# Optimization experiments

Hardware: AMD Instinct MI355X
Metric: run time of the kernel (lower is better)

## Reference

```python
import jax, jax.numpy as jnp
import numpy as np

N = 100000; E = 1600000; G = 2000; S = 40; MAXP = 50
IN = 64; F = 128; H = 4; HD = F // H; FFN = 8 * F
EPS = 1e-5; BN_EPS = 1e-5

def _ln(x, g, b):
    m = jnp.mean(x, -1, keepdims=True)
    v = jnp.mean((x - m) ** 2, -1, keepdims=True)
    return (x - m) * jax.lax.rsqrt(v + EPS) * g + b

def setup_inputs():
    key = jax.random.key(0)
    ks = jax.random.split(key, 16)
    def lin(k, i, o):
        kw, kb = jax.random.split(k)
        lim = 1.0 / np.sqrt(i)
        return (jax.random.uniform(kw, (i, o), jnp.float32, -lim, lim),
                jax.random.uniform(kb, (o,), jnp.float32, -lim, lim))
    W_gcn, b_gcn = lin(ks[1], IN, F)
    Wq, bq = lin(ks[2], F, F); Wk, bk = lin(ks[3], F, F)
    Wv, bv = lin(ks[4], F, F); Wo, bo = lin(ks[5], F, F)
    W1, b1 = lin(ks[6], F, FFN); W2, b2 = lin(ks[7], FFN, F)
    Wg, bg = lin(ks[8], 2 * F, F)
    ones = lambda: jnp.ones((F,), jnp.float32)
    zeros = lambda: jnp.zeros((F,), jnp.float32)
    return {
        'x': jax.random.normal(ks[0], (N, IN), jnp.float32),
        'edge_index': jax.random.randint(ks[9], (2, E), 0, N),
        'batch': jnp.repeat(jnp.arange(G), N // G),
        'set_batch': jnp.repeat(jnp.arange(S), G // S),
        'W_gcn': W_gcn, 'b_gcn': b_gcn,
        'bn_g': ones(), 'bn_b': zeros(),
        'lnpre_g': ones(), 'lnpre_b': zeros(),
        'Wq': Wq, 'bq': bq, 'Wk': Wk, 'bk': bk, 'Wv': Wv, 'bv': bv, 'Wo': Wo, 'bo': bo,
        'ln1_g': ones(), 'ln1_b': zeros(),
        'W1': W1, 'b1': b1, 'W2': W2, 'b2': b2,
        'ln2_g': ones(), 'ln2_b': zeros(),
        'Wg': Wg, 'bg': bg,
    }

def _forward(x, W_gcn, b_gcn, bn_g, bn_b, lnpre_g, lnpre_b, Wq, bq, Wk, bk, Wv, bv, Wo, bo, ln1_g, ln1_b, W1, b1, W2, b2, ln2_g, ln2_b, Wg, bg, edge_index, batch, set_batch):
    row, col = edge_index[0], edge_index[1]
    # GCNConv, improved=True -> self-loop weight 2.0 (PyG gcn_norm)
    xw = x @ W_gcn                                              # [N,F]
    deg = jax.ops.segment_sum(jnp.ones(E, xw.dtype), col, N) + 2.0
    dinv = jax.lax.rsqrt(deg)
    norm = dinv[row] * dinv[col]                                # [E]
    agg = jax.ops.segment_sum(xw[row] * norm[:, None], col, N)  # scatter-add to targets
    h = agg + (2.0 * dinv * dinv)[:, None] * xw + b_gcn
    # BatchNorm1d eval (running_mean=0, running_var=1) + ReLU; dropout is identity in eval
    h = jax.nn.relu(h * jax.lax.rsqrt(jnp.asarray(1.0 + BN_EPS, h.dtype)) * bn_g + bn_b)
    # global mean pool per graph
    cnt_g = jax.ops.segment_sum(jnp.ones(N, h.dtype), batch, G)
    z = jax.ops.segment_sum(h, batch, G) / cnt_g[:, None]       # [G,F]
    # to_dense_batch over sets (set_batch is sorted)
    cnt_s = jax.ops.segment_sum(jnp.ones(G, jnp.int32), set_batch, S)
    starts = jnp.cumsum(cnt_s) - cnt_s
    pos = jnp.arange(G) - starts[set_batch]                     # position within set
    zd = jnp.zeros((S, MAXP, F), z.dtype).at[set_batch, pos].set(z)
    mask = jnp.arange(MAXP)[None, :] < cnt_s[:, None]           # [S,MAXP]
    # pre-LN MHA with key_padding_mask
    zn = _ln(zd, lnpre_g, lnpre_b)
    q = (zn @ Wq + bq).reshape(S, MAXP, H, HD)
    k = (zn @ Wk + bk).reshape(S, MAXP, H, HD)
    v = (zn @ Wv + bv).reshape(S, MAXP, H, HD)
    scores = jnp.einsum('sqhd,skhd->shqk', q, k) / np.sqrt(HD)
    scores = jnp.where(mask[:, None, None, :], scores, -1e9)
    attn = jax.nn.softmax(scores, -1)
    o = jnp.einsum('shqk,skhd->sqhd', attn, v).reshape(S, MAXP, F) @ Wo + bo
    zd = _ln(zd + o, ln1_g, ln1_b)
    # FFN block (post-LN residual)
    f = jax.nn.relu(zd @ W1 + b1) @ W2 + b2
    zd = _ln(zd + f, ln2_g, ln2_b)
    # z_dense[mask] ordering == gather via (set_batch, pos); broadcast to nodes
    set_info = zd[set_batch, pos][batch]                        # [N,F]
    # gated fusion
    gate = jax.nn.sigmoid(jnp.concatenate([h, set_info], -1) @ Wg + bg)
    return gate * set_info + (1.0 - gate) * h

def reference(x, edge_index, batch, set_batch, W_gcn, b_gcn, bn_g, bn_b, lnpre_g, lnpre_b, Wq, bq, Wk, bk, Wv, bv, Wo, bo, ln1_g, ln1_b, W1, b1, W2, b2, ln2_g, ln2_b, Wg, bg):
    return _forward(x, W_gcn, b_gcn, bn_g, bn_b, lnpre_g, lnpre_b, Wq, bq, Wk, bk, Wv, bv, Wo, bo, ln1_g, ln1_b, W1, b1, W2, b2, ln2_g, ln2_b, Wg, bg, edge_index, batch, set_batch)
```

## Files before the change

kernel.cpp:

```cpp
#include <hip/hip_runtime.h>
#include <hip/hip_bf16.h>
#include <cstddef>

#define NN 100000
#define NE 1600000
#define NG 2000
#define NS 40
#define INF 64
#define F 128
#define FFN_DIM 1024
#define NB 782
#define BCAP 3072
#define SC_BLOCKS 512
#define SC_CHUNK 3125

using bf16 = __hip_bfloat16;
typedef __attribute__((ext_vector_type(8))) short short8;
typedef __attribute__((ext_vector_type(4))) float f32x4;
typedef __attribute__((ext_vector_type(2))) float f32x2;

__device__ __forceinline__ short f2bs(float f){
    union { bf16 b; short s; } u; u.b = __float2bfloat16(f); return u.s;
}
__device__ __forceinline__ unsigned int pk2(float a, float b){
    return (unsigned int)(unsigned short)f2bs(a) | ((unsigned int)(unsigned short)f2bs(b) << 16);
}

__global__ __launch_bounds__(1024) void k_init(int* __restrict__ bcursor, const float* __restrict__ Wg,
                                               unsigned short* __restrict__ Wgb){
    int t = threadIdx.x;
    if (t < NB) bcursor[t] = t * BCAP;
    for (int i=t; i<16384; i+=1024){
        int k = i >> 7, n = i & 127;
        Wgb[n*128 + k] = (unsigned short)f2bs(Wg[(size_t)k*F + n]);
    }
}

__global__ __launch_bounds__(256) void k_xws(const float* __restrict__ x, const float* __restrict__ W,
                                             const float* __restrict__ dinv, unsigned char* __restrict__ xws8){
    __shared__ short Xs[128*72];
    __shared__ short Ws[128*72];
    int t = threadIdx.x;
    int rowBase = blockIdx.x * 128;
    #pragma unroll
    for (int i=0;i<32;i++){
        int id = i*256+t; int k = id>>7, n = id&127;
        Ws[n*72 + k] = f2bs(W[id]);
    }
    #pragma unroll
    for (int i=0;i<8;i++){
        int id = i*256+t;
        int r = id>>4; int k4 = (id&15)*4;
        int row = rowBase + r; if (row >= NN) row = NN-1;
        float4 v = *(const float4*)&x[(size_t)row*INF + k4];
        *(unsigned int*)&Xs[r*72 + k4]     = pk2(v.x, v.y);
        *(unsigned int*)&Xs[r*72 + k4 + 2] = pk2(v.z, v.w);
    }
    __syncthreads();
    int lane = t & 63, w = t >> 6;
    int lr = lane & 15, quad = lane >> 4;
    f32x4 acc[2][8];
    #pragma unroll
    for (int i=0;i<2;i++)
        #pragma unroll
        for (int j=0;j<8;j++) acc[i][j] = (f32x4){0.f,0.f,0.f,0.f};
    #pragma unroll
    for (int ks=0; ks<2; ++ks){
        int kb = ks*32 + quad*8;
        short8 b0 = *(const short8*)&Xs[((w  )*16 + lr)*72 + kb];
        short8 b1 = *(const short8*)&Xs[((w+4)*16 + lr)*72 + kb];
        #pragma unroll
        for (int mt=0; mt<8; ++mt){
            short8 a = *(const short8*)&Ws[(mt*16 + lr)*72 + kb];
            acc[0][mt] = __builtin_amdgcn_mfma_f32_16x16x32_bf16(a, b0, acc[0][mt], 0, 0, 0);
            acc[1][mt] = __builtin_amdgcn_mfma_f32_16x16x32_bf16(a, b1, acc[1][mt], 0, 0, 0);
        }
    }
    #pragma unroll
    for (int rt=0; rt<2; ++rt){
        int row = rowBase + (w + rt*4)*16 + lr;
        if (row < NN){
            float dv = dinv[row];
            #pragma unroll
            for (int mt=0; mt<8; ++mt){
                int p = __builtin_amdgcn_cvt_pk_fp8_f32(acc[rt][mt][0]*dv, acc[rt][mt][1]*dv, 0, false);
                p     = __builtin_amdgcn_cvt_pk_fp8_f32(acc[rt][mt][2]*dv, acc[rt][mt][3]*dv, p, true);
                *(int*)&xws8[(size_t)row*F + mt*16 + quad*4] = p;
            }
        }
    }
}

__global__ __launch_bounds__(1024) void k_scatter2(const int* __restrict__ ei, int* __restrict__ bcursor,
                                                   int* __restrict__ ebuf){
    __shared__ int lh[NB];
    __shared__ int lb[NB];
    int t = threadIdx.x;
    int base = blockIdx.x * SC_CHUNK;
    for (int b=t; b<NB; b+=1024) lh[b] = 0;
    __syncthreads();
    int rr[4], cc[4];
    #pragma unroll
    for (int q=0;q<4;q++){
        int i = t + q*1024;
        bool v = (i < SC_CHUNK);
        int idx = v ? (base + i) : base;
        rr[q] = ei[idx];
        cc[q] = ei[NE + idx];
        if (v) atomicAdd(&lh[cc[q]>>7], 1);
    }
    __syncthreads();
    for (int b=t; b<NB; b+=1024){
        int n = lh[b];
        lb[b] = n ? atomicAdd(&bcursor[b], n) : 0;
        lh[b] = 0;
    }
    __syncthreads();
    #pragma unroll
    for (int q=0;q<4;q++){
        int i = t + q*1024;
        if (i < SC_CHUNK){
            int b = cc[q] >> 7;
            int rk = atomicAdd(&lh[b], 1);
            ebuf[lb[b] + rk] = (rr[q] << 7) | (cc[q] & 127);
        }
    }
}

__global__ __launch_bounds__(256) void k_sort(const int* __restrict__ ebuf, const int* __restrict__ bcursor,
                                              int* __restrict__ cnt, float* __restrict__ dinv,
                                              int* __restrict__ nstart, int* __restrict__ ebuf2){
    __shared__ int lh[128];
    __shared__ int s[128];
    __shared__ int lcur[128];
    __shared__ int sorted[BCAP];
    int t = threadIdx.x;
    int b = blockIdx.x;
    int e0 = b * BCAP;
    int nE = bcursor[b] - e0;
    if (t < 128) lh[t] = 0;
    __syncthreads();
    for (int i=t; i<nE; i+=256) atomicAdd(&lh[ebuf[e0+i] & 127], 1);
    __syncthreads();
    int c = (t < 128) ? lh[t] : 0;
    if (t < 128) s[t] = c;
    __syncthreads();
    #pragma unroll
    for (int off=1; off<128; off<<=1){
        int v = (t >= off && t < 128) ? s[t-off] : 0;
        __syncthreads();
        if (t < 128) s[t] += v;
        __syncthreads();
    }
    int node = b*128 + t;
    if (t < 128){
        int excl = s[t] - c;
        lcur[t] = excl;
        if (node < NN){
            nstart[node] = e0 + excl;
            cnt[node] = c;
            dinv[node] = rsqrtf((float)c + 2.0f);
        }
    }
    __syncthreads();
    for (int i=t; i<nE; i+=256){
        int v = ebuf[e0 + i];
        int nl = v & 127;
        int rk = atomicAdd(&lcur[nl], 1);
        sorted[rk] = (v >> 7) << 5;
    }
    __syncthreads();
    for (int i=t; i<nE; i+=256) ebuf2[e0 + i] = sorted[i];
}

__global__ __launch_bounds__(256) void k_aggpool(const unsigned char* __restrict__ xws8,
                                                 const int* __restrict__ nstart, const int* __restrict__ cnt,
                                                 const float* __restrict__ dinv, const float* __restrict__ b_gcn,
                                                 const float* __restrict__ bn_g, const float* __restrict__ bn_b,
                                                 const int* __restrict__ ebuf2,
                                                 const float* __restrict__ lnpre_g, const float* __restrict__ lnpre_b,
                                                 float* __restrict__ h, unsigned short* __restrict__ hb,
                                                 float* __restrict__ z, unsigned short* __restrict__ znb){
    __shared__ float zacc[4][128];
    int t = threadIdx.x;
    int lane = t & 63, w = t >> 6;
    int half = lane >> 5, lh = lane & 31;
    int g = blockIdx.x;
    const unsigned int* xw32 = (const unsigned int*)xws8;
    unsigned int* hb32 = (unsigned int*)hb;
    unsigned int* znb32 = (unsigned int*)znb;

    float4 bg4  = *(const float4*)&b_gcn[4*lh];
    float4 bng4 = *(const float4*)&bn_g[4*lh];
    float4 bnb4 = *(const float4*)&bn_b[4*lh];
    const float bns = rsqrtf(1.f + 1e-5f);

    float za0=0.f, za1=0.f, za2=0.f, za3=0.f;

    for (int i = w; i < 50; i += 4){
        int node = g*50 + i;
        int s0n = nstart[node]; int dg = cnt[node]; float dv = dinv[node];
        unsigned int us = xw32[node*32 + lh];
        float a0=0.f, a1=0.f, a2=0.f, a3=0.f;
        int j=0;
        for (; j+8<=dg; j+=8){
            int r0 = ebuf2[s0n+j+0+half];
            int r1 = ebuf2[s0n+j+2+half];
            int r2 = ebuf2[s0n+j+4+half];
            int r3 = ebuf2[s0n+j+6+half];
            unsigned int u0 = xw32[r0 + lh];
            unsigned int u1 = xw32[r1 + lh];
            unsigned int u2 = xw32[r2 + lh];
            unsigned int u3 = xw32[r3 + lh];
            f32x2 l0 = __builtin_amdgcn_cvt_pk_f32_fp8(u0, false);
            f32x2 h0 = __builtin_amdgcn_cvt_pk_f32_fp8(u0, true);
            f32x2 l1 = __builtin_amdgcn_cvt_pk_f32_fp8(u1, false);
            f32x2 h1 = __builtin_amdgcn_cvt_pk_f32_fp8(u1, true);
            f32x2 l2 = __builtin_amdgcn_cvt_pk_f32_fp8(u2, false);
            f32x2 h2 = __builtin_amdgcn_cvt_pk_f32_fp8(u2, true);
            f32x2 l3 = __builtin_amdgcn_cvt_pk_f32_fp8(u3, false);
            f32x2 h3 = __builtin_amdgcn_cvt_pk_f32_fp8(u3, true);
            a0 += (l0.x + l1.x) + (l2.x + l3.x);
            a1 += (l0.y + l1.y) + (l2.y + l3.y);
            a2 += (h0.x + h1.x) + (h2.x + h3.x);
            a3 += (h0.y + h1.y) + (h2.y + h3.y);
        }
        for (; j+2<=dg; j+=2){
            int r0 = ebuf2[s0n+j+half];
            unsigned int u0 = xw32[r0 + lh];
            f32x2 l0 = __builtin_amdgcn_cvt_pk_f32_fp8(u0, false);
            f32x2 h0 = __builtin_amdgcn_cvt_pk_f32_fp8(u0, true);
            a0 += l0.x; a1 += l0.y; a2 += h0.x; a3 += h0.y;
        }
        if (j < dg && half == 0){
            int r0 = ebuf2[s0n+j];
            unsigned int u0 = xw32[r0 + lh];
            f32x2 l0 = __builtin_amdgcn_cvt_pk_f32_fp8(u0, false);
            f32x2 h0 = __builtin_amdgcn_cvt_pk_f32_fp8(u0, true);
            a0 += l0.x; a1 += l0.y; a2 += h0.x; a3 += h0.y;
        }
        a0 += __shfl_xor(a0, 32);
        a1 += __shfl_xor(a1, 32);
        a2 += __shfl_xor(a2, 32);
        a3 += __shfl_xor(a3, 32);
        f32x2 fl = __builtin_amdgcn_cvt_pk_f32_fp8(us, false);
        f32x2 fh = __builtin_amdgcn_cvt_pk_f32_fp8(us, true);
        float p0 = dv*(a0 + 2.f*fl.x) + bg4.x;
        float p1 = dv*(a1 + 2.f*fl.y) + bg4.y;
        float p2 = dv*(a2 + 2.f*fh.x) + bg4.z;
        float p3 = dv*(a3 + 2.f*fh.y) + bg4.w;
        p0 = fmaxf(p0*bns*bng4.x + bnb4.x, 0.f);
        p1 = fmaxf(p1*bns*bng4.y + bnb4.y, 0.f);
        p2 = fmaxf(p2*bns*bng4.z + bnb4.z, 0.f);
        p3 = fmaxf(p3*bns*bng4.w + bnb4.w, 0.f);
        if (half == 0){
            *(float4*)&h[(size_t)node*F + 4*lh] = make_float4(p0,p1,p2,p3);
            *(uint2*)&hb32[(size_t)node*64 + 2*lh] = make_uint2(pk2(p0,p1), pk2(p2,p3));
        }
        za0 += p0; za1 += p1; za2 += p2; za3 += p3;
    }
    if (half == 0)
        *(float4*)&zacc[w][4*lh] = make_float4(za0, za1, za2, za3);
    __syncthreads();
    if (w == 0){
        float4 v0 = *(const float4*)&zacc[0][4*lh];
        float4 v1 = *(const float4*)&zacc[1][4*lh];
        float4 v2 = *(const float4*)&zacc[2][4*lh];
        float4 v3 = *(const float4*)&zacc[3][4*lh];
        float s0 = ((v0.x+v1.x)+(v2.x+v3.x)) / 50.0f;
        float s1 = ((v0.y+v1.y)+(v2.y+v3.y)) / 50.0f;
        float s2 = ((v0.z+v1.z)+(v2.z+v3.z)) / 50.0f;
        float s3 = ((v0.w+v1.w)+(v2.w+v3.w)) / 50.0f;
        if (half == 0)
            *(float4*)&z[(size_t)g*F + 4*lh] = make_float4(s0,s1,s2,s3);
        float s = (s0+s1)+(s2+s3);
        #pragma unroll
        for (int off=1; off<32; off<<=1) s += __shfl_xor(s, off);
        float m = s * (1.f/128.f);
        float d0=s0-m, d1=s1-m, d2=s2-m, d3=s3-m;
        float vv = (d0*d0+d1*d1)+(d2*d2+d3*d3);
        #pragma unroll
        for (int off=1; off<32; off<<=1) vv += __shfl_xor(vv, off);
        float rs = rsqrtf(vv*(1.f/128.f) + 1e-5f);
        float4 lg = *(const float4*)&lnpre_g[4*lh];
        float4 lb = *(const float4*)&lnpre_b[4*lh];
        if (half == 0){
            float o0 = d0*rs*lg.x+lb.x, o1 = d1*rs*lg.y+lb.y;
            float o2 = d2*rs*lg.z+lb.z, o3 = d3*rs*lg.w+lb.w;
            *(uint2*)&znb32[(size_t)g*64 + 2*lh] = make_uint2(pk2(o0,o1), pk2(o2,o3));
        }
    }
}

__global__ __launch_bounds__(256) void k_settf(const unsigned short* __restrict__ znb,
                                               const float* __restrict__ z,
                                               const float* __restrict__ Wq, const float* __restrict__ bq,
                                               const float* __restrict__ Wk, const float* __restrict__ bk,
                                               const float* __restrict__ Wv, const float* __restrict__ bv,
                                               const float* __restrict__ Wo, const float* __restrict__ bo,
                                               const float* __restrict__ ln1_g, const float* __restrict__ ln1_b,
                                               const float* __restrict__ W1, const float* __restrict__ b1,
                                               const float* __restrict__ W2, const float* __restrict__ b2,
                                               const float* __restrict__ ln2_g, const float* __restrict__ ln2_b,
                                               const float* __restrict__ Wgbot, const float* __restrict__ bg,
                                               float* __restrict__ zd2, float* __restrict__ gsi){
    __shared__ __align__(16) char smem[138208];
    short* Bw   = (short*)smem;
    float* Sc   = (float*)smem;
    float* qs   = (float*)(smem + 41600);
    float* ks   = (float*)(smem + 68000);
    float* vs   = (float*)(smem + 94400);
    short* aob  = (short*)(smem + 120800);
    float* zd1f = (float*)(smem + 41600);
    short* zd1b = (short*)(smem + 68000);
    short* f1b  = (short*)(smem + 94400);
    short* zd2b = f1b;

    int t = threadIdx.x;
    int lane = t & 63, w = t >> 6;
    int lr = lane & 15, quad = lane >> 4;
    int s = blockIdx.x;
    const int r0 = s*50;

    {
        int rl = w*16 + lr; if (rl > 49) rl = 49;
        const unsigned short* arow = &znb[(size_t)(r0 + rl)*F];
        for (int zsel=0; zsel<3; ++zsel){
            const float* Wp = (zsel==0)?Wq:(zsel==1)?Wk:Wv;
            const float* bp = (zsel==0)?bq:(zsel==1)?bk:bv;
            float* outp = (zsel==0)?qs:(zsel==1)?ks:vs;
            for (int i=t; i<16384; i+=256){
                int k = i>>7, n = i&127;
                Bw[n*136 + k] = f2bs(Wp[(size_t)k*F + n]);
            }
            __syncthreads();
            f32x4 acc[8];
            #pragma unroll
            for (int j=0;j<8;j++) acc[j] = (f32x4){0.f,0.f,0.f,0.f};
            #pragma unroll
            for (int ks4=0; ks4<4; ++ks4){
                int kb = ks4*32 + quad*8;
                short8 a = *(const short8*)&arow[kb];
                #pragma unroll
                for (int nt=0; nt<8; ++nt){
                    short8 b = *(const short8*)&Bw[(nt*16 + lr)*136 + kb];
                    acc[nt] = __builtin_amdgcn_mfma_f32_16x16x32_bf16(a, b, acc[nt], 0, 0, 0);
                }
            }
            #pragma unroll
            for (int r=0; r<4; ++r){
                int row = w*16 + quad*4 + r;
                if (row < 50){
                    #pragma unroll
                    for (int nt=0; nt<8; ++nt){
                        int col = nt*16 + lr;
                        outp[row*132 + col] = acc[nt][r] + bp[col];
                    }
                }
            }
            __syncthreads();
        }
    }

    {
        int hh = w;
        float* ScH = Sc + hh*50*52;
        int qi = lane;
        if (qi < 50){
            float qreg[32];
            #pragma unroll
            for (int d=0; d<32; ++d) qreg[d] = qs[qi*132 + hh*32 + d];
            for (int ki=0; ki<50; ++ki){
                float acc=0.f;
                #pragma unroll
                for (int d=0; d<32; ++d) acc += qreg[d] * ks[ki*132 + hh*32 + d];
                ScH[qi*52 + ki] = acc * 0.17677669529663687f;
            }
            float m=-1e30f;
            for (int ki=0; ki<50; ++ki) m = fmaxf(m, ScH[qi*52+ki]);
            float sum=0.f;
            for (int ki=0; ki<50; ++ki){ float e=__expf(ScH[qi*52+ki]-m); ScH[qi*52+ki]=e; sum+=e; }
            float inv = 1.f/sum;
            float o[32];
            #pragma unroll
            for (int d=0; d<32; ++d) o[d] = 0.f;
            for (int ki=0; ki<50; ++ki){
                float sc = ScH[qi*52+ki] * inv;
                #pragma unroll
                for (int d=0; d<32; ++d) o[d] += sc * vs[ki*132 + hh*32 + d];
            }
            #pragma unroll
            for (int d=0; d<32; ++d) aob[qi*136 + hh*32 + d] = f2bs(o[d]);
        } else if (qi < 64){
            #pragma unroll
            for (int d=0; d<32; ++d) aob[qi*136 + hh*32 + d] = 0;
        }
    }
    __syncthreads();

    {
        for (int i=t; i<16384; i+=256){
            int k = i>>7, n = i&127;
            Bw[n*136 + k] = f2bs(Wo[(size_t)k*F + n]);
        }
        __syncthreads();
        f32x4 acc[8];
        #pragma unroll
        for (int j=0;j<8;j++) acc[j] = (f32x4){0.f,0.f,0.f,0.f};
        #pragma unroll
        for (int ks4=0; ks4<4; ++ks4){
            int kb = ks4*32 + quad*8;
            short8 a = *(const short8*)&aob[(w*16 + lr)*136 + kb];
            #pragma unroll
            for (int nt=0; nt<8; ++nt){
                short8 b = *(const short8*)&Bw[(nt*16 + lr)*136 + kb];
                acc[nt] = __builtin_amdgcn_mfma_f32_16x16x32_bf16(a, b, acc[nt], 0, 0, 0);
            }
        }
        __syncthreads();
        #pragma unroll
        for (int r=0; r<4; ++r){
            int row = w*16 + quad*4 + r;
            float v[8];
            if (row < 50){
                #pragma unroll
                for (int nt=0; nt<8; ++nt){
                    int col = nt*16 + lr;
                    v[nt] = acc[nt][r] + bo[col] + z[(size_t)(r0+row)*F + col];
                }
            } else {
                #pragma unroll
                for (int nt=0; nt<8; ++nt) v[nt] = 0.f;
            }
            float ssum = 0.f;
            #pragma unroll
            for (int nt=0; nt<8; ++nt) ssum += v[nt];
            #pragma unroll
            for (int off=1; off<16; off<<=1) ssum += __shfl_xor(ssum, off);
            float mean = ssum * (1.f/128.f);
            float var = 0.f;
            float d[8];
            #pragma unroll
            for (int nt=0; nt<8; ++nt){ d[nt] = v[nt]-mean; var += d[nt]*d[nt]; }
            #pragma unroll
            for (int off=1; off<16; off<<=1) var += __shfl_xor(var, off);
            float rsv = rsqrtf(var*(1.f/128.f) + 1e-5f);
            if (row < 50){
                #pragma unroll
                for (int nt=0; nt<8; ++nt){
                    int col = nt*16 + lr;
                    float o = d[nt]*rsv*ln1_g[col] + ln1_b[col];
                    zd1f[row*132 + col] = o;
                    zd1b[row*136 + col] = f2bs(o);
                }
            } else {
                #pragma unroll
                for (int nt=0; nt<8; ++nt) zd1b[row*136 + nt*16 + lr] = 0;
            }
        }
    }
    __syncthreads();

    f32x4 acc2[8];
    #pragma unroll
    for (int j=0;j<8;j++) acc2[j] = (f32x4){0.f,0.f,0.f,0.f};
    for (int c=0; c<8; ++c){
        for (int i=t; i<16384; i+=256){
            int k = i>>7, n = i&127;
            Bw[n*136 + k] = f2bs(W1[(size_t)k*FFN_DIM + c*128 + n]);
        }
        __syncthreads();
        f32x4 a1[8];
        #pragma unroll
        for (int j=0;j<8;j++) a1[j] = (f32x4){0.f,0.f,0.f,0.f};
        #pragma unroll
        for (int ks4=0; ks4<4; ++ks4){
            int kb = ks4*32 + quad*8;
            short8 a = *(const short8*)&zd1b[(w*16 + lr)*136 + kb];
            #pragma unroll
            for (int nt=0; nt<8; ++nt){
                short8 b = *(const short8*)&Bw[(nt*16 + lr)*136 + kb];
                a1[nt] = __builtin_amdgcn_mfma_f32_16x16x32_bf16(a, b, a1[nt], 0, 0, 0);
            }
        }
        #pragma unroll
        for (int r=0; r<4; ++r){
            int row = w*16 + quad*4 + r;
            #pragma unroll
            for (int nt=0; nt<8; ++nt){
                int col = nt*16 + lr;
                f1b[row*136 + col] = f2bs(fmaxf(a1[nt][r] + b1[c*128 + col], 0.f));
            }
        }
        __syncthreads();
        for (int i=t; i<16384; i+=256){
            int k = i>>7, n = i&127;
            Bw[n*136 + k] = f2bs(W2[(size_t)(c*128 + k)*F + n]);
        }
        __syncthreads();
        #pragma unroll
        for (int ks4=0; ks4<4; ++ks4){
            int kb = ks4*32 + quad*8;
            short8 a = *(const short8*)&f1b[(w*16 + lr)*136 + kb];
            #pragma unroll
            for (int nt=0; nt<8; ++nt){
                short8 b = *(const short8*)&Bw[(nt*16 + lr)*136 + kb];
                acc2[nt] = __builtin_amdgcn_mfma_f32_16x16x32_bf16(a, b, acc2[nt], 0, 0, 0);
            }
        }
        __syncthreads();
    }

    {
        #pragma unroll
        for (int r=0; r<4; ++r){
            int row = w*16 + quad*4 + r;
            float v[8];
            if (row < 50){
                #pragma unroll
                for (int nt=0; nt<8; ++nt){
                    int col = nt*16 + lr;
                    v[nt] = acc2[nt][r] + b2[col] + zd1f[row*132 + col];
                }
            } else {
                #pragma unroll
                for (int nt=0; nt<8; ++nt) v[nt] = 0.f;
            }
            float ssum = 0.f;
            #pragma unroll
            for (int nt=0; nt<8; ++nt) ssum += v[nt];
            #pragma unroll
            for (int off=1; off<16; off<<=1) ssum += __shfl_xor(ssum, off);
            float mean = ssum * (1.f/128.f);
            float var = 0.f;
            float d[8];
            #pragma unroll
            for (int nt=0; nt<8; ++nt){ d[nt] = v[nt]-mean; var += d[nt]*d[nt]; }
            #pragma unroll
            for (int off=1; off<16; off<<=1) var += __shfl_xor(var, off);
            float rsv = rsqrtf(var*(1.f/128.f) + 1e-5f);
            if (row < 50){
                #pragma unroll
                for (int nt=0; nt<8; ++nt){
                    int col = nt*16 + lr;
                    float o = d[nt]*rsv*ln2_g[col] + ln2_b[col];
                    zd2[(size_t)(r0+row)*F + col] = o;
                    zd2b[row*136 + col] = f2bs(o);
                }
            } else {
                #pragma unroll
                for (int nt=0; nt<8; ++nt) zd2b[row*136 + nt*16 + lr] = 0;
            }
        }
        for (int i=t; i<16384; i+=256){
            int k = i>>7, n = i&127;
            Bw[n*136 + k] = f2bs(Wgbot[(size_t)k*F + n]);
        }
        __syncthreads();
        f32x4 ag[8];
        #pragma unroll
        for (int j=0;j<8;j++) ag[j] = (f32x4){0.f,0.f,0.f,0.f};
        #pragma unroll
        for (int ks4=0; ks4<4; ++ks4){
            int kb = ks4*32 + quad*8;
            short8 a = *(const short8*)&zd2b[(w*16 + lr)*136 + kb];
            #pragma unroll
            for (int nt=0; nt<8; ++nt){
                short8 b = *(const short8*)&Bw[(nt*16 + lr)*136 + kb];
                ag[nt] = __builtin_amdgcn_mfma_f32_16x16x32_bf16(a, b, ag[nt], 0, 0, 0);
            }
        }
        #pragma unroll
        for (int r=0; r<4; ++r){
            int row = w*16 + quad*4 + r;
            if (row < 50){
                #pragma unroll
                for (int nt=0; nt<8; ++nt){
                    int col = nt*16 + lr;
                    gsi[(size_t)(r0+row)*F + col] = ag[nt][r] + bg[col];
                }
            }
        }
    }
}

__global__ __launch_bounds__(256) void k_gate_mfma(const float* __restrict__ h,
                                                   const unsigned short* __restrict__ hb,
                                                   const unsigned short* __restrict__ Wgb,
                                                   const float* __restrict__ gsi, const float* __restrict__ zd2,
                                                   float* __restrict__ out){
    int t = threadIdx.x;
    int lane = t & 63, w = t >> 6;
    int lr = lane & 15, quad = lane >> 4;
    int mrow0 = blockIdx.x*64 + w*16;
    f32x4 acc[8];
    #pragma unroll
    for (int j=0;j<8;j++) acc[j] = (f32x4){0.f,0.f,0.f,0.f};
    #pragma unroll
    for (int ks=0; ks<4; ++ks){
        int kb = ks*32 + quad*8;
        int row = mrow0 + lr;
        if (row >= NN) row = NN-1;
        short8 a = *(const short8*)&hb[(size_t)row*F + kb];
        #pragma unroll
        for (int nt=0; nt<8; ++nt){
            short8 b = *(const short8*)&Wgb[(size_t)(nt*16 + lr)*128 + kb];
            acc[nt] = __builtin_amdgcn_mfma_f32_16x16x32_bf16(a, b, acc[nt], 0, 0, 0);
        }
    }
    #pragma unroll
    for (int r=0; r<4; ++r){
        int row = mrow0 + quad*4 + r;
        if (row >= NN) continue;
        int g = row / 50;
        const float* gs = &gsi[(size_t)g*F];
        const float* zs = &zd2[(size_t)g*F];
        const float* hr = &h[(size_t)row*F];
        float* orow = &out[(size_t)row*F];
        #pragma unroll
        for (int nt=0; nt<8; ++nt){
            int col = nt*16 + lr;
            float L = acc[nt][r] + gs[col];
            float gate = 1.f/(1.f + __expf(-L));
            orow[col] = gate*zs[col] + (1.f-gate)*hr[col];
        }
    }
}

extern "C" void kernel_launch(void* const* d_in, const int* in_sizes, int n_in,
                              void* d_out, int out_size, void* d_ws, size_t ws_size,
                              hipStream_t stream) {
    const float* x      = (const float*)d_in[0];
    const int*   ei     = (const int*)d_in[1];
    const float* W_gcn  = (const float*)d_in[4];
    const float* b_gcn  = (const float*)d_in[5];
    const float* bn_g   = (const float*)d_in[6];
    const float* bn_b   = (const float*)d_in[7];
    const float* lnpre_g= (const float*)d_in[8];
    const float* lnpre_b= (const float*)d_in[9];
    const float* Wq     = (const float*)d_in[10];
    const float* bq     = (const float*)d_in[11];
    const float* Wk     = (const float*)d_in[12];
    const float* bk     = (const float*)d_in[13];
    const float* Wv     = (const float*)d_in[14];
    const float* bv     = (const float*)d_in[15];
    const float* Wo     = (const float*)d_in[16];
    const float* bo     = (const float*)d_in[17];
    const float* ln1_g  = (const float*)d_in[18];
    const float* ln1_b  = (const float*)d_in[19];
    const float* W1     = (const float*)d_in[20];
    const float* b1     = (const float*)d_in[21];
    const float* W2     = (const float*)d_in[22];
    const float* b2     = (const float*)d_in[23];
    const float* ln2_g  = (const float*)d_in[24];
    const float* ln2_b  = (const float*)d_in[25];
    const float* Wg     = (const float*)d_in[26];
    const float* bg     = (const float*)d_in[27];
    float* out = (float*)d_out;
    char* ws = (char*)d_ws;

    size_t o = 0;
    unsigned char* xws8 = (unsigned char*)(ws + o); o += (size_t)NN*F;
    float* h     = (float*)(ws + o); o += (size_t)NN*F*4;
    unsigned short* hb = (unsigned short*)(ws + o); o += (size_t)NN*F*2;
    int*   cnt   = (int*)(ws + o);   o += (size_t)NN*4;
    int*   nstart= (int*)(ws + o);   o += (size_t)NN*4;
    int*   ebuf  = (int*)(ws + o);   o += (size_t)NB*BCAP*4;
    int*   ebuf2 = (int*)(ws + o);   o += (size_t)NB*BCAP*4;
    float* dinv  = (float*)(ws + o); o += (size_t)NN*4;
    int*   bcursor=(int*)(ws + o);   o += 1024*4;
    unsigned short* Wgb = (unsigned short*)(ws + o); o += 16384*2;
    float* z     = (float*)(ws + o); o += (size_t)NG*F*4;
    unsigned short* znb = (unsigned short*)(ws + o); o += (size_t)NG*F*2;
    float* zd2   = (float*)(ws + o); o += (size_t)NG*F*4;
    float* gsi   = (float*)(ws + o); o += (size_t)NG*F*4;

    k_init<<<1, 1024, 0, stream>>>(bcursor, Wg, Wgb);
    k_scatter2<<<SC_BLOCKS, 1024, 0, stream>>>(ei, bcursor, ebuf);
    k_sort<<<NB, 256, 0, stream>>>(ebuf, bcursor, cnt, dinv, nstart, ebuf2);
    k_xws<<<(NN+127)/128, 256, 0, stream>>>(x, W_gcn, dinv, xws8);
    k_aggpool<<<NG, 256, 0, stream>>>(xws8, nstart, cnt, dinv, b_gcn, bn_g, bn_b, ebuf2,
                                      lnpre_g, lnpre_b, h, hb, z, znb);

    k_settf<<<NS, 256, 0, stream>>>(znb, z, Wq, bq, Wk, bk, Wv, bv, Wo, bo,
                                    ln1_g, ln1_b, W1, b1, W2, b2, ln2_g, ln2_b,
                                    Wg + (size_t)F*F, bg, zd2, gsi);

    k_gate_mfma<<<(NN+63)/64, 256, 0, stream>>>(h, hb, Wgb, gsi, zd2, out);
}
```

Baseline: 388.5 us.

## Pre-convert transformer weights to bf16 once and read them directly in set transformer

Adds extra blocks to the xws kernel that convert and transpose all set-transformer weights (Wq/Wk/Wv/Wo/W1/W2/Wg) to bf16 in global memory once. The 40-block set-transformer kernel then reads MFMA B operands straight from global/L2 instead of converting each weight into shared memory per block, which removes many syncthreads and redundant fp32 loads. The init kernel is replaced by a memset, with bucket offsets added inside scatter. The cost is uncoalesced-ish global reads for B fragments and extra work in the xws launch.

```diff
diff --git a/kernel.cpp b/kernel.cpp
--- a/kernel.cpp
+++ b/kernel.cpp
@@ -13,6 +13,8 @@
 #define BCAP 3072
 #define SC_BLOCKS 512
 #define SC_CHUNK 3125
+#define NXB 782
+#define NWB 72
 
 using bf16 = __hip_bfloat16;
 typedef __attribute__((ext_vector_type(8))) short short8;
@@ -26,21 +28,41 @@
     return (unsigned int)(unsigned short)f2bs(a) | ((unsigned int)(unsigned short)f2bs(b) << 16);
 }
 
-__global__ __launch_bounds__(1024) void k_init(int* __restrict__ bcursor, const float* __restrict__ Wg,
-                                               unsigned short* __restrict__ Wgb){
+__global__ __launch_bounds__(256) void k_xws(const float* __restrict__ x, const float* __restrict__ W,
+                                             const float* __restrict__ dinv, unsigned char* __restrict__ xws8,
+                                             const float* __restrict__ Wq, const float* __restrict__ Wk,
+                                             const float* __restrict__ Wv, const float* __restrict__ Wo,
+                                             const float* __restrict__ W1, const float* __restrict__ W2,
+                                             const float* __restrict__ Wg,
+                                             unsigned short* __restrict__ Wqb, unsigned short* __restrict__ Wkb,
+                                             unsigned short* __restrict__ Wvb, unsigned short* __restrict__ Wob,
+                                             unsigned short* __restrict__ W1b, unsigned short* __restrict__ W2b,
+                                             unsigned short* __restrict__ Wgb, unsigned short* __restrict__ Wgbotb){
     int t = threadIdx.x;
-    if (t < NB) bcursor[t] = t * BCAP;
-    for (int i=t; i<16384; i+=1024){
-        int k = i >> 7, n = i & 127;
-        Wgb[n*128 + k] = (unsigned short)f2bs(Wg[(size_t)k*F + n]);
-    }
-}
-
-__global__ __launch_bounds__(256) void k_xws(const float* __restrict__ x, const float* __restrict__ W,
-                                             const float* __restrict__ dinv, unsigned char* __restrict__ xws8){
+    if (blockIdx.x >= NXB){
+        int wt = (blockIdx.x - NXB)*256 + t;
+        const int ws = NWB*256;
+        for (int i=wt; i<16384; i+=ws){
+            int k = i>>7, n = i&127;
+            Wqb[n*128+k]    = (unsigned short)f2bs(Wq[(size_t)k*F+n]);
+            Wkb[n*128+k]    = (unsigned short)f2bs(Wk[(size_t)k*F+n]);
+            Wvb[n*128+k]    = (unsigned short)f2bs(Wv[(size_t)k*F+n]);
+            Wob[n*128+k]    = (unsigned short)f2bs(Wo[(size_t)k*F+n]);
+            Wgb[n*128+k]    = (unsigned short)f2bs(Wg[(size_t)k*F+n]);
+            Wgbotb[n*128+k] = (unsigned short)f2bs(Wg[(size_t)(F+k)*F+n]);
+        }
+        for (int i=wt; i<131072; i+=ws){
+            int k = i>>10, n = i&1023;
+            W1b[(size_t)n*128+k] = (unsigned short)f2bs(W1[(size_t)k*FFN_DIM+n]);
+        }
+        for (int i=wt; i<131072; i+=ws){
+            int n = i>>10, k = i&1023;
+            W2b[(size_t)n*1024+k] = (unsigned short)f2bs(W2[(size_t)k*F+n]);
+        }
+        return;
+    }
     __shared__ short Xs[128*72];
     __shared__ short Ws[128*72];
-    int t = threadIdx.x;
     int rowBase = blockIdx.x * 128;
     #pragma unroll
     for (int i=0;i<32;i++){
@@ -112,7 +134,7 @@
     __syncthreads();
     for (int b=t; b<NB; b+=1024){
         int n = lh[b];
-        lb[b] = n ? atomicAdd(&bcursor[b], n) : 0;
+        lb[b] = n ? (b*BCAP + atomicAdd(&bcursor[b], n)) : 0;
         lh[b] = 0;
     }
     __syncthreads();
@@ -137,7 +159,7 @@
     int t = threadIdx.x;
     int b = blockIdx.x;
     int e0 = b * BCAP;
-    int nE = bcursor[b] - e0;
+    int nE = bcursor[b];
     if (t < 128) lh[t] = 0;
     __syncthreads();
     for (int i=t; i<nE; i+=256) atomicAdd(&lh[ebuf[e0+i] & 127], 1);
@@ -292,20 +314,21 @@
     }
 }
 
-__global__ __launch_bounds__(256) void k_settf(const unsigned short* __restrict__ znb,
-                                               const float* __restrict__ z,
-                                               const float* __restrict__ Wq, const float* __restrict__ bq,
-                                               const float* __restrict__ Wk, const float* __restrict__ bk,
-                                               const float* __restrict__ Wv, const float* __restrict__ bv,
-                                               const float* __restrict__ Wo, const float* __restrict__ bo,
-                                               const float* __restrict__ ln1_g, const float* __restrict__ ln1_b,
-                                               const float* __restrict__ W1, const float* __restrict__ b1,
-                                               const float* __restrict__ W2, const float* __restrict__ b2,
-                                               const float* __restrict__ ln2_g, const float* __restrict__ ln2_b,
-                                               const float* __restrict__ Wgbot, const float* __restrict__ bg,
-                                               float* __restrict__ zd2, float* __restrict__ gsi){
+__global__ __launch_bounds__(256) void k_settf2(const unsigned short* __restrict__ znb,
+                                                const float* __restrict__ z,
+                                                const unsigned short* __restrict__ Wqb,
+                                                const unsigned short* __restrict__ Wkb,
+                                                const unsigned short* __restrict__ Wvb,
+                                                const float* __restrict__ bq, const float* __restrict__ bk,
+                                                const float* __restrict__ bv,
+                                                const unsigned short* __restrict__ Wob, const float* __restrict__ bo,
+                                                const float* __restrict__ ln1_g, const float* __restrict__ ln1_b,
+                                                const unsigned short* __restrict__ W1b, const float* __restrict__ b1,
+                                                const unsigned short* __restrict__ W2b, const float* __restrict__ b2,
+                                                const float* __restrict__ ln2_g, const float* __restrict__ ln2_b,
+                                                const unsigned short* __restrict__ Wgbotb, const float* __restrict__ bg,
+                                                float* __restrict__ zd2, float* __restrict__ gsi){
     __shared__ __align__(16) char smem[138208];
-    short* Bw   = (short*)smem;
     float* Sc   = (float*)smem;
     float* qs   = (float*)(smem + 41600);
     float* ks   = (float*)(smem + 68000);
@@ -326,14 +349,9 @@
         int rl = w*16 + lr; if (rl > 49) rl = 49;
         const unsigned short* arow = &znb[(size_t)(r0 + rl)*F];
         for (int zsel=0; zsel<3; ++zsel){
-            const float* Wp = (zsel==0)?Wq:(zsel==1)?Wk:Wv;
+            const unsigned short* B = (zsel==0)?Wqb:(zsel==1)?Wkb:Wvb;
             const float* bp = (zsel==0)?bq:(zsel==1)?bk:bv;
             float* outp = (zsel==0)?qs:(zsel==1)?ks:vs;
-            for (int i=t; i<16384; i+=256){
-                int k = i>>7, n = i&127;
-                Bw[n*136 + k] = f2bs(Wp[(size_t)k*F + n]);
-            }
-            __syncthreads();
             f32x4 acc[8];
             #pragma unroll
             for (int j=0;j<8;j++) acc[j] = (f32x4){0.f,0.f,0.f,0.f};
@@ -343,7 +361,7 @@
                 short8 a = *(const short8*)&arow[kb];
                 #pragma unroll
                 for (int nt=0; nt<8; ++nt){
-                    short8 b = *(const short8*)&Bw[(nt*16 + lr)*136 + kb];
+                    short8 b = *(const short8*)&B[(size_t)(nt*16 + lr)*128 + kb];
                     acc[nt] = __builtin_amdgcn_mfma_f32_16x16x32_bf16(a, b, acc[nt], 0, 0, 0);
                 }
             }
@@ -358,9 +376,9 @@
                     }
                 }
             }
-            __syncthreads();
-        }
-    }
+        }
+    }
+    __syncthreads();
 
     {
         int hh = w;
@@ -399,11 +417,6 @@
     __syncthreads();
 
     {
-        for (int i=t; i<16384; i+=256){
-            int k = i>>7, n = i&127;
-            Bw[n*136 + k] = f2bs(Wo[(size_t)k*F + n]);
-        }
-        __syncthreads();
         f32x4 acc[8];
         #pragma unroll
         for (int j=0;j<8;j++) acc[j] = (f32x4){0.f,0.f,0.f,0.f};
@@ -413,11 +426,10 @@
             short8 a = *(const short8*)&aob[(w*16 + lr)*136 + kb];
             #pragma unroll
             for (int nt=0; nt<8; ++nt){
-                short8 b = *(const short8*)&Bw[(nt*16 + lr)*136 + kb];
+                short8 b = *(const short8*)&Wob[(size_t)(nt*16 + lr)*128 + kb];
                 acc[nt] = __builtin_amdgcn_mfma_f32_16x16x32_bf16(a, b, acc[nt], 0, 0, 0);
             }
         }
-        __syncthreads();
         #pragma unroll
         for (int r=0; r<4; ++r){
             int row = w*16 + quad*4 + r;
@@ -465,11 +477,6 @@
     #pragma unroll
     for (int j=0;j<8;j++) acc2[j] = (f32x4){0.f,0.f,0.f,0.f};
     for (int c=0; c<8; ++c){
-        for (int i=t; i<16384; i+=256){
-            int k = i>>7, n = i&127;
-            Bw[n*136 + k] = f2bs(W1[(size_t)k*FFN_DIM + c*128 + n]);
-        }
-        __syncthreads();
         f32x4 a1[8];
         #pragma unroll
         for (int j=0;j<8;j++) a1[j] = (f32x4){0.f,0.f,0.f,0.f};
@@ -479,7 +486,7 @@
             short8 a = *(const short8*)&zd1b[(w*16 + lr)*136 + kb];
             #pragma unroll
             for (int nt=0; nt<8; ++nt){
-                short8 b = *(const short8*)&Bw[(nt*16 + lr)*136 + kb];
+                short8 b = *(const short8*)&W1b[(size_t)(c*128 + nt*16 + lr)*128 + kb];
                 a1[nt] = __builtin_amdgcn_mfma_f32_16x16x32_bf16(a, b, a1[nt], 0, 0, 0);
             }
         }
@@ -493,18 +500,13 @@
             }
         }
         __syncthreads();
-        for (int i=t; i<16384; i+=256){
-            int k = i>>7, n = i&127;
-            Bw[n*136 + k] = f2bs(W2[(size_t)(c*128 + k)*F + n]);
-        }
-        __syncthreads();
         #pragma unroll
         for (int ks4=0; ks4<4; ++ks4){
             int kb = ks4*32 + quad*8;
             short8 a = *(const short8*)&f1b[(w*16 + lr)*136 + kb];
             #pragma unroll
             for (int nt=0; nt<8; ++nt){
-                short8 b = *(const short8*)&Bw[(nt*16 + lr)*136 + kb];
+                short8 b = *(const short8*)&W2b[(size_t)(nt*16 + lr)*1024 + c*128 + kb];
                 acc2[nt] = __builtin_amdgcn_mfma_f32_16x16x32_bf16(a, b, acc2[nt], 0, 0, 0);
             }
         }
@@ -552,10 +554,6 @@
                 for (int nt=0; nt<8; ++nt) zd2b[row*136 + nt*16 + lr] = 0;
             }
         }
-        for (int i=t; i<16384; i+=256){
-            int k = i>>7, n = i&127;
-            Bw[n*136 + k] = f2bs(Wgbot[(size_t)k*F + n]);
-        }
         __syncthreads();
         f32x4 ag[8];
         #pragma unroll
@@ -566,7 +564,7 @@
             short8 a = *(const short8*)&zd2b[(w*16 + lr)*136 + kb];
             #pragma unroll
             for (int nt=0; nt<8; ++nt){
-                short8 b = *(const short8*)&Bw[(nt*16 + lr)*136 + kb];
+                short8 b = *(const short8*)&Wgbotb[(size_t)(nt*16 + lr)*128 + kb];
                 ag[nt] = __builtin_amdgcn_mfma_f32_16x16x32_bf16(a, b, ag[nt], 0, 0, 0);
             }
         }
@@ -669,22 +667,31 @@
     int*   ebuf2 = (int*)(ws + o);   o += (size_t)NB*BCAP*4;
     float* dinv  = (float*)(ws + o); o += (size_t)NN*4;
     int*   bcursor=(int*)(ws + o);   o += 1024*4;
-    unsigned short* Wgb = (unsigned short*)(ws + o); o += 16384*2;
+    unsigned short* Wgb    = (unsigned short*)(ws + o); o += 16384*2;
+    unsigned short* Wqb    = (unsigned short*)(ws + o); o += 16384*2;
+    unsigned short* Wkb    = (unsigned short*)(ws + o); o += 16384*2;
+    unsigned short* Wvb    = (unsigned short*)(ws + o); o += 16384*2;
+    unsigned short* Wob    = (unsigned short*)(ws + o); o += 16384*2;
+    unsigned short* Wgbotb = (unsigned short*)(ws + o); o += 16384*2;
+    unsigned short* W1b = (unsigned short*)(ws + o); o += (size_t)131072*2;
+    unsigned short* W2b = (unsigned short*)(ws + o); o += (size_t)131072*2;
     float* z     = (float*)(ws + o); o += (size_t)NG*F*4;
     unsigned short* znb = (unsigned short*)(ws + o); o += (size_t)NG*F*2;
     float* zd2   = (float*)(ws + o); o += (size_t)NG*F*4;
     float* gsi   = (float*)(ws + o); o += (size_t)NG*F*4;
 
-    k_init<<<1, 1024, 0, stream>>>(bcursor, Wg, Wgb);
+    hipMemsetAsync(bcursor, 0, (size_t)NB*4, stream);
     k_scatter2<<<SC_BLOCKS, 1024, 0, stream>>>(ei, bcursor, ebuf);
     k_sort<<<NB, 256, 0, stream>>>(ebuf, bcursor, cnt, dinv, nstart, ebuf2);
-    k_xws<<<(NN+127)/128, 256, 0, stream>>>(x, W_gcn, dinv, xws8);
+    k_xws<<<NXB + NWB, 256, 0, stream>>>(x, W_gcn, dinv, xws8,
+                                         Wq, Wk, Wv, Wo, W1, W2, Wg,
+                                         Wqb, Wkb, Wvb, Wob, W1b, W2b, Wgb, Wgbotb);
     k_aggpool<<<NG, 256, 0, stream>>>(xws8, nstart, cnt, dinv, b_gcn, bn_g, bn_b, ebuf2,
                                       lnpre_g, lnpre_b, h, hb, z, znb);
 
-    k_settf<<<NS, 256, 0, stream>>>(znb, z, Wq, bq, Wk, bk, Wv, bv, Wo, bo,
-                                    ln1_g, ln1_b, W1, b1, W2, b2, ln2_g, ln2_b,
-                                    Wg + (size_t)F*F, bg, zd2, gsi);
+    k_settf2<<<NS, 256, 0, stream>>>(znb, z, Wqb, Wkb, Wvb, bq, bk, bv,
+                                     Wob, bo, ln1_g, ln1_b, W1b, b1, W2b, b2,
+                                     ln2_g, ln2_b, Wgbotb, bg, zd2, gsi);
 
     k_gate_mfma<<<(NN+63)/64, 256, 0, stream>>>(h, hb, Wgb, gsi, zd2, out);
 }
```

Result: faster. 373.4 us (-3.9%).
